# Kernel optimization log

Measured on AMD Instinct MI355X. Metric: run time of the kernel, lower is better.

The kernel has to match this reference:

```python
import jax, jax.numpy as jnp
import numpy as np

N_NODES = 100000
N_EDGES = 1600000
IN_CH, HID, N_CLS = 768, 256, 8


def setup_inputs() -> dict:
    key = jax.random.key(0)
    k1, k2, k3, k4 = jax.random.split(key, 4)
    x = jax.random.normal(k1, (N_NODES, IN_CH), dtype=jnp.float32)
    edge_index = jax.random.randint(k2, (2, N_EDGES), 0, N_NODES, dtype=jnp.int64)
    # Glorot-ish init scaled for stability
    W1 = jax.random.normal(k3, (IN_CH, HID), dtype=jnp.float32) * (1.0 / np.sqrt(IN_CH))
    b1 = jnp.zeros((HID,), dtype=jnp.float32)
    W2 = jax.random.normal(k4, (HID, N_CLS), dtype=jnp.float32) * (1.0 / np.sqrt(HID))
    b2 = jnp.zeros((N_CLS,), dtype=jnp.float32)
    return {"x": x, "edge_index": edge_index, "W1": W1, "b1": b1, "W2": W2, "b2": b2}


def _gcn_norm(edge_index, num_nodes):
    # Add self-loops (PyG GCNConv default) and compute symmetric normalization.
    loops = jnp.arange(num_nodes, dtype=edge_index.dtype)
    row = jnp.concatenate([edge_index[0], loops])  # source nodes
    col = jnp.concatenate([edge_index[1], loops])  # target nodes
    ones = jnp.ones(col.shape[0], dtype=jnp.float32)
    deg = jax.ops.segment_sum(ones, col, num_segments=num_nodes)
    dinv = jnp.where(deg > 0, jax.lax.rsqrt(deg), 0.0)
    norm = dinv[row] * dinv[col]  # [E + N]
    return row, col, norm


def _gcn_conv(x, row, col, norm, W, b):
    h = x @ W                      # [N, out] dense transform first (out <= in)
    msg = h[row] * norm[:, None]    # gather + scale, [E+N, out]
    agg = jax.ops.segment_sum(msg, col, num_segments=x.shape[0])  # scatter-add
    return agg + b


def reference(x, edge_index, W1, b1, W2, b2):
    row, col, norm = _gcn_norm(edge_index, x.shape[0])
    h = _gcn_conv(x, row, col, norm, W1, b1)
    h = jax.nn.relu(h)
    # dropout is identity at eval (training=False)
    out = _gcn_conv(h, row, col, norm, W2, b2)
    return out
```

## Files before the change

kernel.cpp:

```cpp
#include <hip/hip_runtime.h>
#include <hip/hip_bf16.h>


#define NN 100000
#define NE 1600000
#define INC 768
#define HID 256
#define NCLS 8
#define DMAX 64

typedef short bf16x8 __attribute__((ext_vector_type(8)));
typedef float f32x4 __attribute__((ext_vector_type(4)));

__device__ __forceinline__ unsigned short f2bf(float f) {
  __hip_bfloat16 h = __float2bfloat16(f);
  return *reinterpret_cast<unsigned short*>(&h);
}
__device__ __forceinline__ float bf2f(unsigned short h) {
  return __uint_as_float(((unsigned int)h) << 16);
}

__global__ __launch_bounds__(256) void k_fillpad(const int* __restrict__ ei,
                                                 int* __restrict__ cnt,
                                                 int* __restrict__ srcidx) {
  int e = blockIdx.x * 256 + threadIdx.x;
  if (e >= NE) return;
  int r = ei[e];
  int c = ei[NE + e];
  int slot = atomicAdd(&cnt[c], 1);
  if (slot < DMAX) srcidx[(long)c * DMAX + slot] = r;
}
__global__ __launch_bounds__(256) void k_dinv(const int* __restrict__ cnt, float* __restrict__ dinv) {
  int i = blockIdx.x * 256 + threadIdx.x;
  if (i < NN) dinv[i] = rsqrtf((float)cnt[i] + 1.0f);
}

__global__ __launch_bounds__(256) void k_w1t(const float* __restrict__ W1, unsigned short* __restrict__ w1t) {
  int t = blockIdx.x * 256 + threadIdx.x;
  if (t >= INC * HID) return;
  int k = t / HID, n = t % HID;
  w1t[n * INC + k] = f2bf(W1[t]);
}

__global__ __launch_bounds__(512) void k_gemm1(const float* __restrict__ x,
                                               const unsigned short* __restrict__ w1t,
                                               unsigned short* __restrict__ h1) {
  __shared__ char smem[49152];
  unsigned short* As = (unsigned short*)smem;
  unsigned short* Bs = (unsigned short*)(smem + 16384);
  const int tid = threadIdx.x;
  const int lane = tid & 63;
  const int wid = tid >> 6;
  const int wm = wid >> 2;
  const int wn = wid & 3;
  const long bm = blockIdx.x;

  const int ar0 = tid >> 3, as7 = tid & 7;
  const int ar1 = (tid + 512) >> 3;
  long arow0 = bm * 128 + ar0; if (arow0 > NN - 1) arow0 = NN - 1;
  long arow1 = bm * 128 + ar1; if (arow1 > NN - 1) arow1 = NN - 1;
  const float* gA0 = x + arow0 * INC + as7 * 8;
  const float* gA1 = x + arow1 * INC + as7 * 8;
  const int aoff0 = (ar0 << 7) | ((as7 ^ (ar0 & 7)) << 4);
  const int aoff1 = (ar1 << 7) | ((as7 ^ (ar1 & 7)) << 4);

  f32x4 acc[4][4];
#pragma unroll
  for (int m = 0; m < 4; m++)
#pragma unroll
    for (int n = 0; n < 4; n++) acc[m][n] = (f32x4){0.f, 0.f, 0.f, 0.f};

  float4 Pa, Pb, Pc, Pd, Qa, Qb, Qc, Qd;
  uint4 rb0, rb1, rb2, rb3;

#define LOAD_ASET(Va, Vb, Vc, Vd, KT)             \
  do {                                            \
    Va = *(const float4*)(gA0 + (KT));            \
    Vb = *(const float4*)(gA0 + (KT) + 4);        \
    Vc = *(const float4*)(gA1 + (KT));            \
    Vd = *(const float4*)(gA1 + (KT) + 4);        \
  } while (0)
#define LOAD_B(KT)                                                                         \
  do {                                                                                     \
    rb0 = *(const uint4*)(w1t + (long)(tid >> 3) * INC + (KT) + (tid & 7) * 8);            \
    rb1 = *(const uint4*)(w1t + (long)((tid + 512) >> 3) * INC + (KT) + (tid & 7) * 8);    \
    rb2 = *(const uint4*)(w1t + (long)((tid + 1024) >> 3) * INC + (KT) + (tid & 7) * 8);   \
    rb3 = *(const uint4*)(w1t + (long)((tid + 1536) >> 3) * INC + (KT) + (tid & 7) * 8);   \
  } while (0)
#define WRITE_ASET(Va, Vb, Vc, Vd)                                                         \
  do {                                                                                     \
    union { unsigned short us[8]; uint4 v; } u;                                            \
    u.us[0] = f2bf(Va.x); u.us[1] = f2bf(Va.y); u.us[2] = f2bf(Va.z);                      \
    u.us[3] = f2bf(Va.w); u.us[4] = f2bf(Vb.x); u.us[5] = f2bf(Vb.y);                      \
    u.us[6] = f2bf(Vb.z); u.us[7] = f2bf(Vb.w);                                            \
    *(uint4*)((char*)As + aoff0) = u.v;                                                    \
    u.us[0] = f2bf(Vc.x); u.us[1] = f2bf(Vc.y); u.us[2] = f2bf(Vc.z);                      \
    u.us[3] = f2bf(Vc.w); u.us[4] = f2bf(Vd.x); u.us[5] = f2bf(Vd.y);                      \
    u.us[6] = f2bf(Vd.z); u.us[7] = f2bf(Vd.w);                                            \
    *(uint4*)((char*)As + aoff1) = u.v;                                                    \
  } while (0)
#define WRITE_B()                                                                          \
  do {                                                                                     \
    int r0 = tid >> 3, s7 = tid & 7;                                                       \
    *(uint4*)((char*)Bs + ((r0 << 7) | ((s7 ^ (r0 & 7)) << 4))) = rb0;                     \
    int r1 = (tid + 512) >> 3;                                                             \
    *(uint4*)((char*)Bs + ((r1 << 7) | ((s7 ^ (r1 & 7)) << 4))) = rb1;                     \
    int r2 = (tid + 1024) >> 3;                                                            \
    *(uint4*)((char*)Bs + ((r2 << 7) | ((s7 ^ (r2 & 7)) << 4))) = rb2;                     \
    int r3 = (tid + 1536) >> 3;                                                            \
    *(uint4*)((char*)Bs + ((r3 << 7) | ((s7 ^ (r3 & 7)) << 4))) = rb3;                     \
  } while (0)
#define MFMA_STEP()                                                                        \
  do {                                                                                     \
    _Pragma("unroll")                                                                      \
    for (int half = 0; half < 2; half++) {                                                 \
      bf16x8 af[4], bff[4];                                                                \
      int j = (half << 2) + (lane >> 4);                                                   \
      _Pragma("unroll")                                                                    \
      for (int m = 0; m < 4; m++) {                                                        \
        int row = wm * 64 + m * 16 + (lane & 15);                                          \
        af[m] = *(const bf16x8*)((const char*)As + ((row << 7) | ((j ^ (row & 7)) << 4))); \
      }                                                                                    \
      _Pragma("unroll")                                                                    \
      for (int n = 0; n < 4; n++) {                                                        \
        int row = wn * 64 + n * 16 + (lane & 15);                                          \
        bff[n] = *(const bf16x8*)((const char*)Bs + ((row << 7) | ((j ^ (row & 7)) << 4)));\
      }                                                                                    \
      _Pragma("unroll")                                                                    \
      for (int m = 0; m < 4; m++)                                                          \
        _Pragma("unroll")                                                                  \
        for (int n = 0; n < 4; n++)                                                        \
          acc[m][n] = __builtin_amdgcn_mfma_f32_16x16x32_bf16(af[m], bff[n], acc[m][n], 0, 0, 0); \
    }                                                                                      \
  } while (0)

  LOAD_ASET(Pa, Pb, Pc, Pd, 0);
  LOAD_B(0);
  LOAD_ASET(Qa, Qb, Qc, Qd, 64);

#pragma unroll 1
  for (int u = 0; u < 6; u++) {
    int kt = u * 128;
    WRITE_ASET(Pa, Pb, Pc, Pd);
    WRITE_B();
    __syncthreads();
    if (kt + 64 < INC) LOAD_B(kt + 64);
    if (kt + 128 < INC) LOAD_ASET(Pa, Pb, Pc, Pd, kt + 128);
    MFMA_STEP();
    __syncthreads();
    WRITE_ASET(Qa, Qb, Qc, Qd);
    WRITE_B();
    __syncthreads();
    if (kt + 128 < INC) LOAD_B(kt + 128);
    if (kt + 192 < INC) LOAD_ASET(Qa, Qb, Qc, Qd, kt + 192);
    MFMA_STEP();
    __syncthreads();
  }
#undef LOAD_ASET
#undef LOAD_B
#undef WRITE_ASET
#undef WRITE_B
#undef MFMA_STEP

  unsigned short* Os = (unsigned short*)smem;
#pragma unroll
  for (int chunk = 0; chunk < 2; chunk++) {
    if (wm == chunk) {
#pragma unroll
      for (int m = 0; m < 4; m++)
#pragma unroll
        for (int n = 0; n < 4; n++) {
          int lrow = m * 16 + ((lane >> 4) << 2);
          int lcol = wn * 64 + n * 16 + (lane & 15);
#pragma unroll
          for (int r = 0; r < 4; r++)
            Os[(lrow + r) * 264 + lcol] = f2bf(acc[m][n][r]);
        }
    }
    __syncthreads();
    {
      int r = tid >> 3, s = tid & 7;
      long grow = bm * 128 + chunk * 64 + r;
      if (grow < NN) {
        unsigned short* dst = h1 + grow * HID;
#pragma unroll
        for (int i = 0; i < 4; i++) {
          int seg = s + i * 8;
          *(uint4*)(dst + seg * 8) = *(const uint4*)((const char*)Os + (long)r * 528 + seg * 16);
        }
      }
    }
    __syncthreads();
  }
}

__global__ __launch_bounds__(256) void k_agg1(const unsigned short* __restrict__ h1,
                                              const float* __restrict__ dinv,
                                              const int* __restrict__ cnt,
                                              const int* __restrict__ srcidx,
                                              const float* __restrict__ b1,
                                              const float* __restrict__ W2,
                                              float* __restrict__ h2) {
  int w = (int)((blockIdx.x * 256 + threadIdx.x) >> 6);
  int lane = threadIdx.x & 63;
  if (w >= NN) return;
  float di = dinv[w];
  int c4 = lane << 2;
  const unsigned short* hb = h1 + c4;
  ushort4 hv = *(const ushort4*)(hb + (long)w * HID);
  float self = di * di;
  float a0 = self * bf2f(hv.x), a1 = self * bf2f(hv.y);
  float a2 = self * bf2f(hv.z), a3 = self * bf2f(hv.w);
  int deg = cnt[w];
  if (deg > DMAX) deg = DMAX;
  const int* sr = srcidx + (long)w * DMAX;
  int e = 0;
  for (; e + 8 <= deg; e += 8) {
    int4 s0 = *(const int4*)(sr + e);
    int4 s1 = *(const int4*)(sr + e + 4);
    float w0 = di * dinv[s0.x], w1 = di * dinv[s0.y];
    float w2 = di * dinv[s0.z], w3 = di * dinv[s0.w];
    float w4 = di * dinv[s1.x], w5 = di * dinv[s1.y];
    float w6 = di * dinv[s1.z], w7 = di * dinv[s1.w];
    ushort4 g0 = *(const ushort4*)(hb + (long)s0.x * HID);
    ushort4 g1 = *(const ushort4*)(hb + (long)s0.y * HID);
    ushort4 g2 = *(const ushort4*)(hb + (long)s0.z * HID);
    ushort4 g3 = *(const ushort4*)(hb + (long)s0.w * HID);
    ushort4 g4 = *(const ushort4*)(hb + (long)s1.x * HID);
    ushort4 g5 = *(const ushort4*)(hb + (long)s1.y * HID);
    ushort4 g6 = *(const ushort4*)(hb + (long)s1.z * HID);
    ushort4 g7 = *(const ushort4*)(hb + (long)s1.w * HID);
    a0 += w0 * bf2f(g0.x) + w1 * bf2f(g1.x) + w2 * bf2f(g2.x) + w3 * bf2f(g3.x) +
          w4 * bf2f(g4.x) + w5 * bf2f(g5.x) + w6 * bf2f(g6.x) + w7 * bf2f(g7.x);
    a1 += w0 * bf2f(g0.y) + w1 * bf2f(g1.y) + w2 * bf2f(g2.y) + w3 * bf2f(g3.y) +
          w4 * bf2f(g4.y) + w5 * bf2f(g5.y) + w6 * bf2f(g6.y) + w7 * bf2f(g7.y);
    a2 += w0 * bf2f(g0.z) + w1 * bf2f(g1.z) + w2 * bf2f(g2.z) + w3 * bf2f(g3.z) +
          w4 * bf2f(g4.z) + w5 * bf2f(g5.z) + w6 * bf2f(g6.z) + w7 * bf2f(g7.z);
    a3 += w0 * bf2f(g0.w) + w1 * bf2f(g1.w) + w2 * bf2f(g2.w) + w3 * bf2f(g3.w) +
          w4 * bf2f(g4.w) + w5 * bf2f(g5.w) + w6 * bf2f(g6.w) + w7 * bf2f(g7.w);
  }
  for (; e < deg; e++) {
    int src = sr[e];
    float ws = di * dinv[src];
    ushort4 g = *(const ushort4*)(hb + (long)src * HID);
    a0 += ws * bf2f(g.x); a1 += ws * bf2f(g.y);
    a2 += ws * bf2f(g.z); a3 += ws * bf2f(g.w);
  }
  float4 bv = *(const float4*)(b1 + c4);
  float v0 = a0 + bv.x; v0 = v0 > 0.f ? v0 : 0.f;
  float v1 = a1 + bv.y; v1 = v1 > 0.f ? v1 : 0.f;
  float v2 = a2 + bv.z; v2 = v2 > 0.f ? v2 : 0.f;
  float v3 = a3 + bv.w; v3 = v3 > 0.f ? v3 : 0.f;
  const float4* wp = (const float4*)(W2 + ((long)c4 << 3));
  float4 r0a = wp[0], r0b = wp[1], r1a = wp[2], r1b = wp[3];
  float4 r2a = wp[4], r2b = wp[5], r3a = wp[6], r3b = wp[7];
  float p[8];
  p[0] = v0 * r0a.x + v1 * r1a.x + v2 * r2a.x + v3 * r3a.x;
  p[1] = v0 * r0a.y + v1 * r1a.y + v2 * r2a.y + v3 * r3a.y;
  p[2] = v0 * r0a.z + v1 * r1a.z + v2 * r2a.z + v3 * r3a.z;
  p[3] = v0 * r0a.w + v1 * r1a.w + v2 * r2a.w + v3 * r3a.w;
  p[4] = v0 * r0b.x + v1 * r1b.x + v2 * r2b.x + v3 * r3b.x;
  p[5] = v0 * r0b.y + v1 * r1b.y + v2 * r2b.y + v3 * r3b.y;
  p[6] = v0 * r0b.z + v1 * r1b.z + v2 * r2b.z + v3 * r3b.z;
  p[7] = v0 * r0b.w + v1 * r1b.w + v2 * r2b.w + v3 * r3b.w;
#pragma unroll
  for (int c = 0; c < 8; c++)
#pragma unroll
    for (int off = 1; off < 64; off <<= 1) p[c] += __shfl_xor(p[c], off, 64);
  if (lane < 8) {
    float o = p[0];
    o = (lane == 1) ? p[1] : o;
    o = (lane == 2) ? p[2] : o;
    o = (lane == 3) ? p[3] : o;
    o = (lane == 4) ? p[4] : o;
    o = (lane == 5) ? p[5] : o;
    o = (lane == 6) ? p[6] : o;
    o = (lane == 7) ? p[7] : o;
    h2[(long)w * NCLS + lane] = o;
  }
}

__global__ __launch_bounds__(256) void k_agg2(const float* __restrict__ h2,
                                              const float* __restrict__ dinv,
                                              const int* __restrict__ cnt,
                                              const int* __restrict__ srcidx,
                                              const float* __restrict__ b2,
                                              float* __restrict__ out) {
  long t = (long)blockIdx.x * 256 + threadIdx.x;
  long i = t >> 3;
  int c = (int)(t & 7);
  if (i >= NN) return;
  float di = dinv[i];
  float s = di * di * h2[i * NCLS + c];
  int deg = cnt[i];
  if (deg > DMAX) deg = DMAX;
  const int* sr = srcidx + i * DMAX;
  int e = 0;
  for (; e + 8 <= deg; e += 8) {
    int4 s0 = *(const int4*)(sr + e);
    int4 s1 = *(const int4*)(sr + e + 4);
    float g0 = dinv[s0.x] * h2[(long)s0.x * NCLS + c];
    float g1 = dinv[s0.y] * h2[(long)s0.y * NCLS + c];
    float g2 = dinv[s0.z] * h2[(long)s0.z * NCLS + c];
    float g3 = dinv[s0.w] * h2[(long)s0.w * NCLS + c];
    float g4 = dinv[s1.x] * h2[(long)s1.x * NCLS + c];
    float g5 = dinv[s1.y] * h2[(long)s1.y * NCLS + c];
    float g6 = dinv[s1.z] * h2[(long)s1.z * NCLS + c];
    float g7 = dinv[s1.w] * h2[(long)s1.w * NCLS + c];
    s += di * (g0 + g1 + g2 + g3 + g4 + g5 + g6 + g7);
  }
  for (; e < deg; e++) {
    int src = sr[e];
    s += di * dinv[src] * h2[(long)src * NCLS + c];
  }
  out[i * NCLS + c] = s + b2[c];
}

extern "C" void kernel_launch(void* const* d_in, const int* in_sizes, int n_in,
                              void* d_out, int out_size, void* d_ws, size_t ws_size,
                              hipStream_t stream) {
  (void)in_sizes; (void)n_in; (void)out_size; (void)ws_size;
  const float* x  = (const float*)d_in[0];
  const int*   ei = (const int*)d_in[1];
  const float* W1 = (const float*)d_in[2];
  const float* b1 = (const float*)d_in[3];
  const float* W2 = (const float*)d_in[4];
  const float* b2 = (const float*)d_in[5];
  float* out = (float*)d_out;
  char* ws = (char*)d_ws;

  unsigned short* h1   = (unsigned short*)(ws + 0L);
  float* h2            = (float*)(ws + 51200000L);
  float* dinv          = (float*)(ws + 54400000L);
  int*   cnt           = (int*)(ws + 54800000L);
  int*   srcidx        = (int*)(ws + 55200000L);
  unsigned short* w1t  = (unsigned short*)(ws + 80800000L);

  hipMemsetAsync(cnt, 0, NN * sizeof(int), stream);
  k_fillpad<<<(NE + 255) / 256, 256, 0, stream>>>(ei, cnt, srcidx);
  k_dinv<<<(NN + 255) / 256, 256, 0, stream>>>(cnt, dinv);
  k_w1t<<<(INC * HID + 255) / 256, 256, 0, stream>>>(W1, w1t);
  k_gemm1<<<782, 512, 0, stream>>>(x, w1t, h1);
  k_agg1<<<(NN * 64 + 255) / 256, 256, 0, stream>>>(h1, dinv, cnt, srcidx, b1, W2, h2);
  k_agg2<<<(NN * NCLS + 255) / 256, 256, 0, stream>>>(h2, dinv, cnt, srcidx, b2, out);
}
```

Baseline: 433.3 us.

## Pre-scale node features by dinv to remove per-edge dinv gathers

The symmetric normalization is factored so that source-side dinv is applied once per node: the GEMM epilogue multiplies rows by dinv, and agg1 stores h2 pre-scaled by dinv. The aggregation kernels then sum neighbor rows directly and apply the destination dinv once at the end, which removes the random dinv gathers and per-edge multiplies. Rounding changes slightly because scaling now happens before the bf16 conversion.

New measurement: 407.2 us. 1.06x faster.

```diff
diff --git a/kernel.cpp b/kernel.cpp
--- a/kernel.cpp
+++ b/kernel.cpp
@@ -44,7 +44,8 @@
 
 __global__ __launch_bounds__(512) void k_gemm1(const float* __restrict__ x,
                                                const unsigned short* __restrict__ w1t,
-                                               unsigned short* __restrict__ h1) {
+                                               const float* __restrict__ dinv,
+                                               unsigned short* __restrict__ h1s) {
   __shared__ char smem[49152];
   unsigned short* As = (unsigned short*)smem;
   unsigned short* Bs = (unsigned short*)(smem + 16384);
@@ -167,22 +168,30 @@
   for (int chunk = 0; chunk < 2; chunk++) {
     if (wm == chunk) {
 #pragma unroll
-      for (int m = 0; m < 4; m++)
+      for (int m = 0; m < 4; m++) {
+        int grow0 = (int)(bm * 128) + chunk * 64 + m * 16 + ((lane >> 4) << 2);
+        float dv[4];
+#pragma unroll
+        for (int r = 0; r < 4; r++) {
+          int gr = grow0 + r;
+          dv[r] = dinv[gr < NN ? gr : NN - 1];
+        }
 #pragma unroll
         for (int n = 0; n < 4; n++) {
           int lrow = m * 16 + ((lane >> 4) << 2);
           int lcol = wn * 64 + n * 16 + (lane & 15);
 #pragma unroll
           for (int r = 0; r < 4; r++)
-            Os[(lrow + r) * 264 + lcol] = f2bf(acc[m][n][r]);
+            Os[(lrow + r) * 264 + lcol] = f2bf(acc[m][n][r] * dv[r]);
         }
+      }
     }
     __syncthreads();
     {
       int r = tid >> 3, s = tid & 7;
       long grow = bm * 128 + chunk * 64 + r;
       if (grow < NN) {
-        unsigned short* dst = h1 + grow * HID;
+        unsigned short* dst = h1s + grow * HID;
 #pragma unroll
         for (int i = 0; i < 4; i++) {
           int seg = s + i * 8;
@@ -194,23 +203,21 @@
   }
 }
 
-__global__ __launch_bounds__(256) void k_agg1(const unsigned short* __restrict__ h1,
+__global__ __launch_bounds__(256) void k_agg1(const unsigned short* __restrict__ h1s,
                                               const float* __restrict__ dinv,
                                               const int* __restrict__ cnt,
                                               const int* __restrict__ srcidx,
                                               const float* __restrict__ b1,
                                               const float* __restrict__ W2,
-                                              float* __restrict__ h2) {
+                                              float* __restrict__ h2s) {
   int w = (int)((blockIdx.x * 256 + threadIdx.x) >> 6);
   int lane = threadIdx.x & 63;
   if (w >= NN) return;
   float di = dinv[w];
   int c4 = lane << 2;
-  const unsigned short* hb = h1 + c4;
+  const unsigned short* hb = h1s + c4;
   ushort4 hv = *(const ushort4*)(hb + (long)w * HID);
-  float self = di * di;
-  float a0 = self * bf2f(hv.x), a1 = self * bf2f(hv.y);
-  float a2 = self * bf2f(hv.z), a3 = self * bf2f(hv.w);
+  float a0 = bf2f(hv.x), a1 = bf2f(hv.y), a2 = bf2f(hv.z), a3 = bf2f(hv.w);
   int deg = cnt[w];
   if (deg > DMAX) deg = DMAX;
   const int* sr = srcidx + (long)w * DMAX;
@@ -218,10 +225,6 @@
   for (; e + 8 <= deg; e += 8) {
     int4 s0 = *(const int4*)(sr + e);
     int4 s1 = *(const int4*)(sr + e + 4);
-    float w0 = di * dinv[s0.x], w1 = di * dinv[s0.y];
-    float w2 = di * dinv[s0.z], w3 = di * dinv[s0.w];
-    float w4 = di * dinv[s1.x], w5 = di * dinv[s1.y];
-    float w6 = di * dinv[s1.z], w7 = di * dinv[s1.w];
     ushort4 g0 = *(const ushort4*)(hb + (long)s0.x * HID);
     ushort4 g1 = *(const ushort4*)(hb + (long)s0.y * HID);
     ushort4 g2 = *(const ushort4*)(hb + (long)s0.z * HID);
@@ -230,27 +233,26 @@
     ushort4 g5 = *(const ushort4*)(hb + (long)s1.y * HID);
     ushort4 g6 = *(const ushort4*)(hb + (long)s1.z * HID);
     ushort4 g7 = *(const ushort4*)(hb + (long)s1.w * HID);
-    a0 += w0 * bf2f(g0.x) + w1 * bf2f(g1.x) + w2 * bf2f(g2.x) + w3 * bf2f(g3.x) +
-          w4 * bf2f(g4.x) + w5 * bf2f(g5.x) + w6 * bf2f(g6.x) + w7 * bf2f(g7.x);
-    a1 += w0 * bf2f(g0.y) + w1 * bf2f(g1.y) + w2 * bf2f(g2.y) + w3 * bf2f(g3.y) +
-          w4 * bf2f(g4.y) + w5 * bf2f(g5.y) + w6 * bf2f(g6.y) + w7 * bf2f(g7.y);
-    a2 += w0 * bf2f(g0.z) + w1 * bf2f(g1.z) + w2 * bf2f(g2.z) + w3 * bf2f(g3.z) +
-          w4 * bf2f(g4.z) + w5 * bf2f(g5.z) + w6 * bf2f(g6.z) + w7 * bf2f(g7.z);
-    a3 += w0 * bf2f(g0.w) + w1 * bf2f(g1.w) + w2 * bf2f(g2.w) + w3 * bf2f(g3.w) +
-          w4 * bf2f(g4.w) + w5 * bf2f(g5.w) + w6 * bf2f(g6.w) + w7 * bf2f(g7.w);
+    a0 += bf2f(g0.x) + bf2f(g1.x) + bf2f(g2.x) + bf2f(g3.x) +
+          bf2f(g4.x) + bf2f(g5.x) + bf2f(g6.x) + bf2f(g7.x);
+    a1 += bf2f(g0.y) + bf2f(g1.y) + bf2f(g2.y) + bf2f(g3.y) +
+          bf2f(g4.y) + bf2f(g5.y) + bf2f(g6.y) + bf2f(g7.y);
+    a2 += bf2f(g0.z) + bf2f(g1.z) + bf2f(g2.z) + bf2f(g3.z) +
+          bf2f(g4.z) + bf2f(g5.z) + bf2f(g6.z) + bf2f(g7.z);
+    a3 += bf2f(g0.w) + bf2f(g1.w) + bf2f(g2.w) + bf2f(g3.w) +
+          bf2f(g4.w) + bf2f(g5.w) + bf2f(g6.w) + bf2f(g7.w);
   }
   for (; e < deg; e++) {
     int src = sr[e];
-    float ws = di * dinv[src];
     ushort4 g = *(const ushort4*)(hb + (long)src * HID);
-    a0 += ws * bf2f(g.x); a1 += ws * bf2f(g.y);
-    a2 += ws * bf2f(g.z); a3 += ws * bf2f(g.w);
+    a0 += bf2f(g.x); a1 += bf2f(g.y);
+    a2 += bf2f(g.z); a3 += bf2f(g.w);
   }
   float4 bv = *(const float4*)(b1 + c4);
-  float v0 = a0 + bv.x; v0 = v0 > 0.f ? v0 : 0.f;
-  float v1 = a1 + bv.y; v1 = v1 > 0.f ? v1 : 0.f;
-  float v2 = a2 + bv.z; v2 = v2 > 0.f ? v2 : 0.f;
-  float v3 = a3 + bv.w; v3 = v3 > 0.f ? v3 : 0.f;
+  float v0 = di * a0 + bv.x; v0 = v0 > 0.f ? v0 : 0.f;
+  float v1 = di * a1 + bv.y; v1 = v1 > 0.f ? v1 : 0.f;
+  float v2 = di * a2 + bv.z; v2 = v2 > 0.f ? v2 : 0.f;
+  float v3 = di * a3 + bv.w; v3 = v3 > 0.f ? v3 : 0.f;
   const float4* wp = (const float4*)(W2 + ((long)c4 << 3));
   float4 r0a = wp[0], r0b = wp[1], r1a = wp[2], r1b = wp[3];
   float4 r2a = wp[4], r2b = wp[5], r3a = wp[6], r3b = wp[7];
@@ -276,11 +278,11 @@
     o = (lane == 5) ? p[5] : o;
     o = (lane == 6) ? p[6] : o;
     o = (lane == 7) ? p[7] : o;
-    h2[(long)w * NCLS + lane] = o;
-  }
-}
-
-__global__ __launch_bounds__(256) void k_agg2(const float* __restrict__ h2,
+    h2s[(long)w * NCLS + lane] = di * o;
+  }
+}
+
+__global__ __launch_bounds__(256) void k_agg2(const float* __restrict__ h2s,
                                               const float* __restrict__ dinv,
                                               const int* __restrict__ cnt,
                                               const int* __restrict__ srcidx,
@@ -291,7 +293,7 @@
   int c = (int)(t & 7);
   if (i >= NN) return;
   float di = dinv[i];
-  float s = di * di * h2[i * NCLS + c];
+  float s = h2s[i * NCLS + c];
   int deg = cnt[i];
   if (deg > DMAX) deg = DMAX;
   const int* sr = srcidx + i * DMAX;
@@ -299,21 +301,16 @@
   for (; e + 8 <= deg; e += 8) {
     int4 s0 = *(const int4*)(sr + e);
     int4 s1 = *(const int4*)(sr + e + 4);
-    float g0 = dinv[s0.x] * h2[(long)s0.x * NCLS + c];
-    float g1 = dinv[s0.y] * h2[(long)s0.y * NCLS + c];
-    float g2 = dinv[s0.z] * h2[(long)s0.z * NCLS + c];
-    float g3 = dinv[s0.w] * h2[(long)s0.w * NCLS + c];
-    float g4 = dinv[s1.x] * h2[(long)s1.x * NCLS + c];
-    float g5 = dinv[s1.y] * h2[(long)s1.y * NCLS + c];
-    float g6 = dinv[s1.z] * h2[(long)s1.z * NCLS + c];
-    float g7 = dinv[s1.w] * h2[(long)s1.w * NCLS + c];
-    s += di * (g0 + g1 + g2 + g3 + g4 + g5 + g6 + g7);
+    float g0 = h2s[(long)s0.x * NCLS + c], g1 = h2s[(long)s0.y * NCLS + c];
+    float g2 = h2s[(long)s0.z * NCLS + c], g3 = h2s[(long)s0.w * NCLS + c];
+    float g4 = h2s[(long)s1.x * NCLS + c], g5 = h2s[(long)s1.y * NCLS + c];
+    float g6 = h2s[(long)s1.z * NCLS + c], g7 = h2s[(long)s1.w * NCLS + c];
+    s += g0 + g1 + g2 + g3 + g4 + g5 + g6 + g7;
   }
   for (; e < deg; e++) {
-    int src = sr[e];
-    s += di * dinv[src] * h2[(long)src * NCLS + c];
-  }
-  out[i * NCLS + c] = s + b2[c];
+    s += h2s[(long)sr[e] * NCLS + c];
+  }
+  out[i * NCLS + c] = di * s + b2[c];
 }
 
 extern "C" void kernel_launch(void* const* d_in, const int* in_sizes, int n_in,
@@ -329,8 +326,8 @@
   float* out = (float*)d_out;
   char* ws = (char*)d_ws;
 
-  unsigned short* h1   = (unsigned short*)(ws + 0L);
-  float* h2            = (float*)(ws + 51200000L);
+  unsigned short* h1s  = (unsigned short*)(ws + 0L);
+  float* h2s           = (float*)(ws + 51200000L);
   float* dinv          = (float*)(ws + 54400000L);
   int*   cnt           = (int*)(ws + 54800000L);
   int*   srcidx        = (int*)(ws + 55200000L);
@@ -340,7 +337,7 @@
   k_fillpad<<<(NE + 255) / 256, 256, 0, stream>>>(ei, cnt, srcidx);
   k_dinv<<<(NN + 255) / 256, 256, 0, stream>>>(cnt, dinv);
   k_w1t<<<(INC * HID + 255) / 256, 256, 0, stream>>>(W1, w1t);
-  k_gemm1<<<782, 512, 0, stream>>>(x, w1t, h1);
-  k_agg1<<<(NN * 64 + 255) / 256, 256, 0, stream>>>(h1, dinv, cnt, srcidx, b1, W2, h2);
-  k_agg2<<<(NN * NCLS + 255) / 256, 256, 0, stream>>>(h2, dinv, cnt, srcidx, b2, out);
-}
+  k_gemm1<<<782, 512, 0, stream>>>(x, w1t, dinv, h1s);
+  k_agg1<<<(NN * 64 + 255) / 256, 256, 0, stream>>>(h1s, dinv, cnt, srcidx, b1, W2, h2s);
+  k_agg2<<<(NN * NCLS + 255) / 256, 256, 0, stream>>>(h2s, dinv, cnt, srcidx, b2, out);
+}
```
